# Kernel optimization log

Measured on AMD Instinct MI355X. Metric: run time of the kernel, lower is better.

## Reference

```python
import jax, jax.numpy as jnp
import numpy as np

B, T, X, E, H, L = 4096, 32, 256, 32, 512, 2  # batch, theta_size, x_size, n_masks, hidden, num_hidden_layers


def _prelu(v, a):
    # PReLU with per-channel slope a (broadcast [E,H] or [B,E,H] vs [B,E,H])
    return jnp.where(v >= 0, v, a * v)


def setup_inputs() -> dict:
    key = jax.random.key(0)
    ks = jax.random.split(key, 12)
    theta = jax.random.normal(ks[0], (B, T), dtype=jnp.float32)
    x = jax.random.normal(ks[1], (B, X), dtype=jnp.float32)
    masks = jax.random.randint(ks[2], (E, T), 0, 2, dtype=jnp.int32)
    masks = masks.at[:, 0].set(1)  # guarantee non-empty subsets
    D = T + X
    s_in = 1.0 / np.sqrt(D)
    s_h = 1.0 / np.sqrt(H)
    # first Linear, split into theta-part and x-part of the weight matrix
    W1t = jax.random.normal(ks[3], (E, T, H), dtype=jnp.float32) * s_in
    W1x = jax.random.normal(ks[4], (E, X, H), dtype=jnp.float32) * s_in
    b1 = jax.random.normal(ks[5], (E, H), dtype=jnp.float32) * s_in
    a1 = jnp.full((E, H), 0.25, dtype=jnp.float32)  # PReLU init
    # num_layers hidden Linear(H,H) + PReLU
    Wh = jax.random.normal(ks[6], (L, E, H, H), dtype=jnp.float32) * s_h
    bh = jax.random.normal(ks[7], (L, E, H), dtype=jnp.float32) * s_h
    ah = jnp.full((L, E, H), 0.25, dtype=jnp.float32)
    # output Linear(H, 1) -> squeeze(-1)
    Wo = jax.random.normal(ks[8], (E, H), dtype=jnp.float32) * s_h
    bo = jax.random.normal(ks[9], (E,), dtype=jnp.float32) * s_h
    return {"theta": theta, "x": x, "masks": masks, "W1t": W1t, "W1x": W1x,
            "b1": b1, "a1": a1, "Wh": Wh, "bh": bh, "ah": ah, "Wo": Wo, "bo": bo}


def reference(theta, x, masks, W1t, W1x, b1, a1, Wh, bh, ah, Wo, bo):
    # theta[..., mask] followed by Linear is equivalent to masking theta per
    # expert and contracting with the full per-expert theta weight block.
    m = masks.astype(theta.dtype)                      # [E, T]
    tm = theta[:, None, :] * m[None, :, :]             # [B, E, T]
    h = (jnp.einsum('bet,eth->beh', tm, W1t)
         + jnp.einsum('bx,exh->beh', x, W1x) + b1)     # [B, E, H]
    h = _prelu(h, a1)
    for i in range(Wh.shape[0]):                       # small fixed layer loop
        h = jnp.einsum('beh,ehk->bek', h, Wh[i]) + bh[i]
        h = _prelu(h, ah[i])
    # Linear(H,1).squeeze(-1), stacked over masks on the last dim -> [B, E]
    return jnp.einsum('beh,eh->be', h, Wo) + bo
```

## Files before the change

### kernel.cpp

```cpp
#include <hip/hip_runtime.h>
#include <stdint.h>

#define B_SZ 4096
#define T_SZ 32
#define X_SZ 256
#define E_SZ 32
#define H_SZ 512
#define BM   64
#define AROW 1040

typedef __attribute__((ext_vector_type(8))) short  short8;
typedef __attribute__((ext_vector_type(4))) float  floatx4;

__device__ __forceinline__ unsigned short f2bf(float f) {
  unsigned u = __float_as_uint(f);
  u += 0x7fffu + ((u >> 16) & 1u);
  return (unsigned short)(u >> 16);
}
__device__ __forceinline__ unsigned pk2(float a, float b) {
  return (unsigned)f2bf(a) | ((unsigned)f2bf(b) << 16);
}

#define LPITCH 524

__global__ __launch_bounds__(256) void prep3_kernel(
    const float* __restrict__ W1t, const float* __restrict__ W1x,
    const int* __restrict__ masks, const float* __restrict__ Wh,
    uint4* __restrict__ wcat, uint4* __restrict__ whf) {
  __shared__ unsigned short lds[32 * LPITCH];
  const int bid = blockIdx.x, t = threadIdx.x;
  const int x   = bid & 7, j = bid >> 3;
  const int q41 = j / 41;
  const int c   = j - q41 * 41;
  const int e   = x * 4 + (3 - q41);
  float4 v[16];
  if (c < 9) {
#pragma unroll
    for (int p = 0; p < 16; ++p) {
      int f  = p * 256 + t;
      int kk = f >> 7, n = (f & 127) * 4;
      int k  = c * 32 + kk;
      if (k < T_SZ) {
        v[p] = *(const float4*)(W1t + ((size_t)e * T_SZ + k) * H_SZ + n);
        float m = (float)masks[e * T_SZ + k];
        v[p].x *= m; v[p].y *= m; v[p].z *= m; v[p].w *= m;
      } else {
        v[p] = *(const float4*)(W1x + ((size_t)e * X_SZ + (k - T_SZ)) * H_SZ + n);
      }
    }
  } else {
    int h = c - 9, le = h >> 4, kt = h & 15;
    const float* base = Wh + (size_t)(le * E_SZ + e) * H_SZ * H_SZ +
                        (size_t)kt * 32 * H_SZ;
#pragma unroll
    for (int p = 0; p < 16; ++p) {
      int f  = p * 256 + t;
      int kk = f >> 7, n = (f & 127) * 4;
      v[p] = *(const float4*)(base + (size_t)kk * H_SZ + n);
    }
  }
#pragma unroll
  for (int p = 0; p < 16; ++p) {
    int f  = p * 256 + t;
    int kk = f >> 7, n = (f & 127) * 4;
    *(uint2*)&lds[kk * LPITCH + n] =
        make_uint2(pk2(v[p].x, v[p].y), pk2(v[p].z, v[p].w));
  }
  __syncthreads();
  uint4* dst = (c < 9)
                   ? (wcat + ((size_t)e * 9 + c) * 2048)
                   : (whf + ((size_t)(((c - 9) >> 4) * E_SZ + e) * 16 +
                             ((c - 9) & 15)) * 2048);
#pragma unroll 2
  for (int p = 0; p < 8; ++p) {
    int u  = p * 256 + t;
    int nb = u >> 6, l = u & 63;
    int n  = nb * 16 + (l & 15);
    int k0 = (l >> 4) * 8;
    unsigned d[4];
#pragma unroll
    for (int jj = 0; jj < 4; ++jj) {
      unsigned lo = lds[(k0 + 2 * jj)     * LPITCH + n];
      unsigned hi = lds[(k0 + 2 * jj + 1) * LPITCH + n];
      d[jj] = lo | (hi << 16);
    }
    dst[u] = make_uint4(d[0], d[1], d[2], d[3]);
  }
}

__global__ __launch_bounds__(512, 4) void mlp_kernel(
    const float* __restrict__ theta, const float* __restrict__ x,
    const short8* __restrict__ wcat, const short8* __restrict__ whf,
    const float* __restrict__ b1, const float* __restrict__ a1,
    const float* __restrict__ bh, const float* __restrict__ ah,
    const float* __restrict__ Wo, const float* __restrict__ bo,
    float* __restrict__ out) {
  __shared__ __align__(16) char smA[BM * AROW];
  const int tid = threadIdx.x;
  const int bid = blockIdx.x;
  const int e   = (bid & 7) * 4 + (bid >> 9);
  const int m0  = ((bid >> 3) & 63) * BM;
  const int w   = tid >> 6, l = tid & 63, l16 = l & 15, quad = l >> 4;

  {
    int r = tid >> 3, c = tid & 7;
    float4 th = *(const float4*)(theta + (size_t)(m0 + r) * T_SZ + c * 4);
    *(uint2*)(smA + r * AROW + c * 8) = make_uint2(pk2(th.x, th.y), pk2(th.z, th.w));
    const float4* xp = (const float4*)(x + (size_t)(m0 + r) * X_SZ);
#pragma unroll
    for (int q = 0; q < 4; ++q) {
      int ch = q * 8 + c;
      float4 a = xp[ch * 2], bv = xp[ch * 2 + 1];
      *(uint4*)(smA + r * AROW + 64 + ch * 16) =
          make_uint4(pk2(a.x, a.y), pk2(a.z, a.w), pk2(bv.x, bv.y), pk2(bv.z, bv.w));
    }
  }
  __syncthreads();

  floatx4 acc[4][4];

  auto gemm = [&](const short8* wbase, int nkt) {
#pragma unroll
    for (int mb = 0; mb < 4; ++mb)
#pragma unroll
      for (int i = 0; i < 4; ++i) acc[mb][i] = (floatx4)(0.f);
    const short8* wp = wbase + w * 256 + l;
    short8 b0[4], b1v[4];
#pragma unroll
    for (int i = 0; i < 4; ++i) b0[i] = wp[i * 64];
    auto step = [&](const short8* bc, int ktt) {
      short8 af[4];
#pragma unroll
      for (int mb = 0; mb < 4; ++mb)
        af[mb] = *(const short8*)(smA + (mb * 16 + l16) * AROW + ktt * 64 + quad * 16);
#pragma unroll
      for (int mb = 0; mb < 4; ++mb)
#pragma unroll
        for (int i = 0; i < 4; ++i)
          acc[mb][i] = __builtin_amdgcn_mfma_f32_16x16x32_bf16(af[mb], bc[i],
                                                               acc[mb][i], 0, 0, 0);
    };
    int kt = 0;
    while (kt + 2 <= nkt) {
#pragma unroll
      for (int i = 0; i < 4; ++i) b1v[i] = wp[(size_t)(kt + 1) * 2048 + i * 64];
      step(b0, kt);
      int k2 = (kt + 2 < nkt) ? kt + 2 : nkt - 1;
#pragma unroll
      for (int i = 0; i < 4; ++i) b0[i] = wp[(size_t)k2 * 2048 + i * 64];
      step(b1v, kt + 1);
      kt += 2;
    }
    if (kt < nkt) step(b0, kt);
  };

  auto epi_store = [&](const float* bias, const float* slope) {
    float bb[4], aa[4];
#pragma unroll
    for (int i = 0; i < 4; ++i) {
      int col = w * 64 + i * 16 + l16;
      bb[i] = bias[col];
      aa[i] = slope[col];
    }
    __syncthreads();
#pragma unroll
    for (int mb = 0; mb < 4; ++mb) {
#pragma unroll
      for (int i = 0; i < 4; ++i) {
        unsigned dw[4];
#pragma unroll
        for (int r = 0; r < 4; ++r) {
          float v = acc[mb][i][r] + bb[i];
          v = v >= 0.f ? v : aa[i] * v;
          float o  = __shfl_xor(v, 1, 64);
          float lo = (l16 & 1) ? o : v;
          float hi = (l16 & 1) ? v : o;
          dw[r] = pk2(lo, hi);
        }
        int col2  = w * 64 + i * 16 + (l16 & ~1);
        int rbase = (l16 & 1) * 2;
#pragma unroll
        for (int rr = 0; rr < 2; ++rr) {
          int row = mb * 16 + quad * 4 + rbase + rr;
          *(unsigned*)(smA + row * AROW + col2 * 2) = dw[rbase + rr];
        }
      }
    }
    __syncthreads();
  };

  gemm(wcat + (size_t)e * 9 * 2048, 9);
  epi_store(b1 + (size_t)e * H_SZ, a1 + (size_t)e * H_SZ);
  gemm(whf + (size_t)e * 16 * 2048, 16);
  epi_store(bh + (size_t)e * H_SZ, ah + (size_t)e * H_SZ);
  gemm(whf + (size_t)(E_SZ + e) * 16 * 2048, 16);
  {
    float bb[4], aa[4], wo[4];
#pragma unroll
    for (int i = 0; i < 4; ++i) {
      int col = w * 64 + i * 16 + l16;
      bb[i] = bh[(size_t)(E_SZ + e) * H_SZ + col];
      aa[i] = ah[(size_t)(E_SZ + e) * H_SZ + col];
      wo[i] = Wo[(size_t)e * H_SZ + col];
    }
    float ps[4][4];
#pragma unroll
    for (int mb = 0; mb < 4; ++mb)
#pragma unroll
      for (int r = 0; r < 4; ++r) ps[mb][r] = 0.f;
#pragma unroll
    for (int mb = 0; mb < 4; ++mb)
#pragma unroll
      for (int i = 0; i < 4; ++i)
#pragma unroll
        for (int r = 0; r < 4; ++r) {
          float v = acc[mb][i][r] + bb[i];
          v = v >= 0.f ? v : aa[i] * v;
          ps[mb][r] += v * wo[i];
        }
#pragma unroll
    for (int d = 1; d < 16; d <<= 1)
#pragma unroll
      for (int mb = 0; mb < 4; ++mb)
#pragma unroll
        for (int r = 0; r < 4; ++r) ps[mb][r] += __shfl_xor(ps[mb][r], d, 64);
    __syncthreads();
    float* scratch = (float*)smA;
    if (l16 == 0) {
#pragma unroll
      for (int mb = 0; mb < 4; ++mb)
#pragma unroll
        for (int r = 0; r < 4; ++r)
          scratch[(mb * 16 + quad * 4 + r) * 8 + w] = ps[mb][r];
    }
    __syncthreads();
    if (tid < BM) {
      float s = 0.f;
#pragma unroll
      for (int ww = 0; ww < 8; ++ww) s += scratch[tid * 8 + ww];
      out[(size_t)(m0 + tid) * E_SZ + e] = s + bo[e];
    }
  }
}

extern "C" void kernel_launch(void* const* d_in, const int* in_sizes, int n_in,
                              void* d_out, int out_size, void* d_ws, size_t ws_size,
                              hipStream_t stream) {
  const float* theta = (const float*)d_in[0];
  const float* x     = (const float*)d_in[1];
  const int*   masks = (const int*)d_in[2];
  const float* W1t   = (const float*)d_in[3];
  const float* W1x   = (const float*)d_in[4];
  const float* b1    = (const float*)d_in[5];
  const float* a1    = (const float*)d_in[6];
  const float* Wh    = (const float*)d_in[7];
  const float* bh    = (const float*)d_in[8];
  const float* ah    = (const float*)d_in[9];
  const float* Wo    = (const float*)d_in[10];
  const float* bo    = (const float*)d_in[11];
  float* out = (float*)d_out;

  uint4* wcat = (uint4*)d_ws;
  uint4* whf  = (uint4*)((char*)d_ws + (size_t)E_SZ * 9 * 2048 * 16);

  prep3_kernel<<<1312, 256, 0, stream>>>(W1t, W1x, masks, Wh, wcat, whf);
  mlp_kernel<<<2048, 512, 0, stream>>>(theta, x, (const short8*)wcat,
                                       (const short8*)whf, b1, a1, bh, ah, Wo, bo,
                                       out);
}
```

Before: 334.4 us.

## Pre-convert inputs to bf16 once, split MLP into four phase launches, template GEMM loop

```diff
diff --git a/kernel.cpp b/kernel.cpp
--- a/kernel.cpp
+++ b/kernel.cpp
@@ -8,6 +8,7 @@
 #define H_SZ 512
 #define BM   64
 #define AROW 1040
+#define D_SZ 288
 
 typedef __attribute__((ext_vector_type(8))) short  short8;
 typedef __attribute__((ext_vector_type(4))) float  floatx4;
@@ -23,16 +24,36 @@
 
 #define LPITCH 524
 
-__global__ __launch_bounds__(256) void prep3_kernel(
+__global__ __launch_bounds__(256) void prep4_kernel(
     const float* __restrict__ W1t, const float* __restrict__ W1x,
     const int* __restrict__ masks, const float* __restrict__ Wh,
-    uint4* __restrict__ wcat, uint4* __restrict__ whf) {
+    const float* __restrict__ theta, const float* __restrict__ x,
+    uint4* __restrict__ wcat, uint4* __restrict__ whf,
+    unsigned short* __restrict__ tx) {
+  const int bid = blockIdx.x, t = threadIdx.x;
+  if (bid >= 1312) {
+    int g = bid - 1312;
+    int r = g * 64 + (t >> 2), c = t & 3;
+    {
+      float4 a = *(const float4*)(theta + (size_t)r * T_SZ + c * 8);
+      float4 b = *(const float4*)(theta + (size_t)r * T_SZ + c * 8 + 4);
+      *(uint4*)(tx + (size_t)r * D_SZ + c * 8) =
+          make_uint4(pk2(a.x, a.y), pk2(a.z, a.w), pk2(b.x, b.y), pk2(b.z, b.w));
+    }
+#pragma unroll
+    for (int j = 0; j < 8; ++j) {
+      float4 a = *(const float4*)(x + (size_t)r * X_SZ + c * 64 + j * 8);
+      float4 b = *(const float4*)(x + (size_t)r * X_SZ + c * 64 + j * 8 + 4);
+      *(uint4*)(tx + (size_t)r * D_SZ + T_SZ + c * 64 + j * 8) =
+          make_uint4(pk2(a.x, a.y), pk2(a.z, a.w), pk2(b.x, b.y), pk2(b.z, b.w));
+    }
+    return;
+  }
   __shared__ unsigned short lds[32 * LPITCH];
-  const int bid = blockIdx.x, t = threadIdx.x;
-  const int x   = bid & 7, j = bid >> 3;
+  const int xcd = bid & 7, j = bid >> 3;
   const int q41 = j / 41;
   const int c   = j - q41 * 41;
-  const int e   = x * 4 + (3 - q41);
+  const int e   = xcd * 4 + (3 - q41);
   float4 v[16];
   if (c < 9) {
 #pragma unroll
@@ -88,71 +109,62 @@
   }
 }
 
+template <int NKT>
+__device__ __forceinline__ void gemm_run(const char* smA, const short8* wp,
+                                         int l16, int quad,
+                                         floatx4 (&acc)[4][4]) {
+#pragma unroll
+  for (int mb = 0; mb < 4; ++mb)
+#pragma unroll
+    for (int i = 0; i < 4; ++i) acc[mb][i] = (floatx4)(0.f);
+  short8 buf[2][4];
+#pragma unroll
+  for (int i = 0; i < 4; ++i) buf[0][i] = wp[i * 64];
+#pragma unroll
+  for (int kt = 0; kt < NKT; ++kt) {
+    int nk = (kt + 1 < NKT) ? kt + 1 : kt;
+    short8* nb = buf[(kt + 1) & 1];
+#pragma unroll
+    for (int i = 0; i < 4; ++i) nb[i] = wp[(size_t)nk * 2048 + i * 64];
+    short8 af[4];
+#pragma unroll
+    for (int mb = 0; mb < 4; ++mb)
+      af[mb] = *(const short8*)(smA + (mb * 16 + l16) * AROW + kt * 64 + quad * 16);
+    const short8* cb = buf[kt & 1];
+#pragma unroll
+    for (int mb = 0; mb < 4; ++mb)
+#pragma unroll
+      for (int i = 0; i < 4; ++i)
+        acc[mb][i] = __builtin_amdgcn_mfma_f32_16x16x32_bf16(af[mb], cb[i],
+                                                             acc[mb][i], 0, 0, 0);
+  }
+}
+
 __global__ __launch_bounds__(512, 4) void mlp_kernel(
-    const float* __restrict__ theta, const float* __restrict__ x,
+    const unsigned short* __restrict__ tx,
     const short8* __restrict__ wcat, const short8* __restrict__ whf,
     const float* __restrict__ b1, const float* __restrict__ a1,
     const float* __restrict__ bh, const float* __restrict__ ah,
     const float* __restrict__ Wo, const float* __restrict__ bo,
-    float* __restrict__ out) {
+    float* __restrict__ out, int phase) {
   __shared__ __align__(16) char smA[BM * AROW];
   const int tid = threadIdx.x;
   const int bid = blockIdx.x;
-  const int e   = (bid & 7) * 4 + (bid >> 9);
-  const int m0  = ((bid >> 3) & 63) * BM;
+  const int e   = (bid & 7) * 4 + phase;
+  const int m0  = (bid >> 3) * BM;
   const int w   = tid >> 6, l = tid & 63, l16 = l & 15, quad = l >> 4;
 
   {
     int r = tid >> 3, c = tid & 7;
-    float4 th = *(const float4*)(theta + (size_t)(m0 + r) * T_SZ + c * 4);
-    *(uint2*)(smA + r * AROW + c * 8) = make_uint2(pk2(th.x, th.y), pk2(th.z, th.w));
-    const float4* xp = (const float4*)(x + (size_t)(m0 + r) * X_SZ);
-#pragma unroll
-    for (int q = 0; q < 4; ++q) {
-      int ch = q * 8 + c;
-      float4 a = xp[ch * 2], bv = xp[ch * 2 + 1];
-      *(uint4*)(smA + r * AROW + 64 + ch * 16) =
-          make_uint4(pk2(a.x, a.y), pk2(a.z, a.w), pk2(bv.x, bv.y), pk2(bv.z, bv.w));
-    }
+    const unsigned short* src = tx + (size_t)(m0 + r) * D_SZ;
+#pragma unroll
+    for (int p = 0; p < 9; ++p)
+      *(uint2*)(smA + r * AROW + 8 * (c + 8 * p)) =
+          *(const uint2*)(src + 4 * (c + 8 * p));
   }
   __syncthreads();
 
   floatx4 acc[4][4];
-
-  auto gemm = [&](const short8* wbase, int nkt) {
-#pragma unroll
-    for (int mb = 0; mb < 4; ++mb)
-#pragma unroll
-      for (int i = 0; i < 4; ++i) acc[mb][i] = (floatx4)(0.f);
-    const short8* wp = wbase + w * 256 + l;
-    short8 b0[4], b1v[4];
-#pragma unroll
-    for (int i = 0; i < 4; ++i) b0[i] = wp[i * 64];
-    auto step = [&](const short8* bc, int ktt) {
-      short8 af[4];
-#pragma unroll
-      for (int mb = 0; mb < 4; ++mb)
-        af[mb] = *(const short8*)(smA + (mb * 16 + l16) * AROW + ktt * 64 + quad * 16);
-#pragma unroll
-      for (int mb = 0; mb < 4; ++mb)
-#pragma unroll
-        for (int i = 0; i < 4; ++i)
-          acc[mb][i] = __builtin_amdgcn_mfma_f32_16x16x32_bf16(af[mb], bc[i],
-                                                               acc[mb][i], 0, 0, 0);
-    };
-    int kt = 0;
-    while (kt + 2 <= nkt) {
-#pragma unroll
-      for (int i = 0; i < 4; ++i) b1v[i] = wp[(size_t)(kt + 1) * 2048 + i * 64];
-      step(b0, kt);
-      int k2 = (kt + 2 < nkt) ? kt + 2 : nkt - 1;
-#pragma unroll
-      for (int i = 0; i < 4; ++i) b0[i] = wp[(size_t)k2 * 2048 + i * 64];
-      step(b1v, kt + 1);
-      kt += 2;
-    }
-    if (kt < nkt) step(b0, kt);
-  };
 
   auto epi_store = [&](const float* bias, const float* slope) {
     float bb[4], aa[4];
@@ -189,11 +201,12 @@
     __syncthreads();
   };
 
-  gemm(wcat + (size_t)e * 9 * 2048, 9);
+  const int woff = w * 256 + l;
+  gemm_run<9>(smA, wcat + (size_t)e * 9 * 2048 + woff, l16, quad, acc);
   epi_store(b1 + (size_t)e * H_SZ, a1 + (size_t)e * H_SZ);
-  gemm(whf + (size_t)e * 16 * 2048, 16);
+  gemm_run<16>(smA, whf + (size_t)e * 16 * 2048 + woff, l16, quad, acc);
   epi_store(bh + (size_t)e * H_SZ, ah + (size_t)e * H_SZ);
-  gemm(whf + (size_t)(E_SZ + e) * 16 * 2048, 16);
+  gemm_run<16>(smA, whf + (size_t)(E_SZ + e) * 16 * 2048 + woff, l16, quad, acc);
   {
     float bb[4], aa[4], wo[4];
 #pragma unroll
@@ -262,9 +275,14 @@
 
   uint4* wcat = (uint4*)d_ws;
   uint4* whf  = (uint4*)((char*)d_ws + (size_t)E_SZ * 9 * 2048 * 16);
-
-  prep3_kernel<<<1312, 256, 0, stream>>>(W1t, W1x, masks, Wh, wcat, whf);
-  mlp_kernel<<<2048, 512, 0, stream>>>(theta, x, (const short8*)wcat,
-                                       (const short8*)whf, b1, a1, bh, ah, Wo, bo,
-                                       out);
-}
+  unsigned short* tx =
+      (unsigned short*)((char*)d_ws + (size_t)E_SZ * 9 * 2048 * 16 +
+                        (size_t)2 * E_SZ * 16 * 2048 * 16);
+
+  prep4_kernel<<<1376, 256, 0, stream>>>(W1t, W1x, masks, Wh, theta, x,
+                                         wcat, whf, tx);
+  for (int p = 0; p < 4; ++p)
+    mlp_kernel<<<512, 512, 0, stream>>>(tx, (const short8*)wcat,
+                                        (const short8*)whf, b1, a1, bh, ah, Wo,
+                                        bo, out, p);
+}
```

Measured after the change: 326.2 us. -2.5%, faster.
